# Kernel tuning notes

Measured on AMD Instinct MI355X. Metric: run time of the kernel, lower is better.

The kernel has to match this reference:

```python
import jax, jax.numpy as jnp
import numpy as np

K_CENTERS = 10
G_CENTERS = 2
EPS = 1e-12  # tf.math.l2_normalize epsilon


def setup_inputs() -> dict:
    key = jax.random.key(0)
    k1, k2, k3 = jax.random.split(key, 3)
    B, H, W, D = 16, 16, 64, 512
    KC = K_CENTERS + G_CENTERS
    feat = jax.random.normal(k1, (B, H, W, D), dtype=jnp.float32)
    cluster_score = jax.random.normal(k2, (B, H, W, KC), dtype=jnp.float32)
    cluster = jax.random.normal(k3, (KC, D), dtype=jnp.float32)
    return {"feat": feat, "cluster_score": cluster_score, "cluster": cluster}


def reference(feat, cluster_score, cluster):
    B, H, W, D = feat.shape
    KC = cluster.shape[0]
    # Softmax over clusters (stable)
    A = jax.nn.softmax(cluster_score, axis=-1)            # [B,H,W,KC]
    # Flatten spatial dims: sum_{s} A[b,s,k] * (feat[b,s,d] - cluster[k,d])
    Af = A.reshape(B, H * W, KC)
    ff = feat.reshape(B, H * W, D)
    # = einsum(A, feat) - (sum_s A)[b,k] * cluster[k,d]  (avoids [B,S,KC,D] intermediate)
    cluster_res = jnp.einsum('bsk,bsd->bkd', Af, ff) - Af.sum(axis=1)[..., None] * cluster[None]
    # GhostVLAD: keep only real clusters
    cluster_res = cluster_res[:, :K_CENTERS, :]           # [B,K,D]
    # L2 normalize over feature dim
    sq = jnp.sum(cluster_res * cluster_res, axis=-1, keepdims=True)
    cluster_l2 = cluster_res * jax.lax.rsqrt(jnp.maximum(sq, EPS))
    return cluster_l2.reshape(B, K_CENTERS * D)
```

## Files before the change

### kernel.cpp

```cpp
#include <hip/hip_runtime.h>


#define B_   16
#define S_   1024
#define D_   512
#define KC_  12
#define K_   10
#define CH_  16
#define SCH_ (S_ / CH_)
#define NT1  512
#define NPAR 4
#define NPX  (SCH_ / NPAR)

__global__ __launch_bounds__(NT1, 2) void vlad_accum(
    const float* __restrict__ feat, const float* __restrict__ score,
    float* __restrict__ part, float* __restrict__ asum_part)
{
    const int bid = blockIdx.x;
    const int b = bid / CH_, c = bid % CH_;
    const int s0 = c * SCH_;
    const int tid = threadIdx.x;
    const int par = tid >> 7;
    const int col = tid & 127;

    __shared__ float  As[SCH_][KC_];
    __shared__ float4 red[NPAR - 1][K_][128];

    float4 w0, w1, w2;
    if (tid < SCH_) {
        const float4* sp = (const float4*)(score + (size_t)(b * S_ + s0 + tid) * KC_);
        w0 = sp[0]; w1 = sp[1]; w2 = sp[2];
    }

    const float4* fp = (const float4*)(feat + (size_t)(b * S_ + s0) * D_) + col;
    float4 v[NPX];
    #pragma unroll
    for (int i = 0; i < NPX; i++)
        v[i] = fp[(size_t)(NPAR * i + par) * (D_ / 4)];

    if (tid < SCH_) {
        float x[KC_] = {w0.x, w0.y, w0.z, w0.w, w1.x, w1.y, w1.z, w1.w,
                        w2.x, w2.y, w2.z, w2.w};
        float m = x[0];
        #pragma unroll
        for (int k = 1; k < KC_; k++) m = fmaxf(m, x[k]);
        float sum = 0.f;
        #pragma unroll
        for (int k = 0; k < KC_; k++) { x[k] = __expf(x[k] - m); sum += x[k]; }
        const float inv = 1.0f / sum;
        #pragma unroll
        for (int k = 0; k < KC_; k++) {
            x[k] *= inv;
            As[tid][k] = x[k];
        }
        #pragma unroll
        for (int k = 0; k < K_; k++) {
            float r = x[k];
            #pragma unroll
            for (int off = 32; off > 0; off >>= 1) r += __shfl_down(r, off, 64);
            if (tid == 0) asum_part[(b * CH_ + c) * K_ + k] = r;
        }
    }
    __syncthreads();

    float acc[K_][4];
    #pragma unroll
    for (int k = 0; k < K_; k++)
        acc[k][0] = acc[k][1] = acc[k][2] = acc[k][3] = 0.f;

    #pragma unroll
    for (int i = 0; i < NPX; i++) {
        const int s = NPAR * i + par;
        const float4 a0 = *(const float4*)&As[s][0];
        const float4 a1 = *(const float4*)&As[s][4];
        const float2 a2 = *(const float2*)&As[s][8];
        const float a[K_] = {a0.x, a0.y, a0.z, a0.w, a1.x, a1.y, a1.z, a1.w,
                             a2.x, a2.y};
        #pragma unroll
        for (int k = 0; k < K_; k++) {
            acc[k][0] += a[k] * v[i].x;
            acc[k][1] += a[k] * v[i].y;
            acc[k][2] += a[k] * v[i].z;
            acc[k][3] += a[k] * v[i].w;
        }
    }

    if (par) {
        #pragma unroll
        for (int k = 0; k < K_; k++)
            red[par - 1][k][col] =
                make_float4(acc[k][0], acc[k][1], acc[k][2], acc[k][3]);
    }
    __syncthreads();
    if (!par) {
        float* pp = part + (((size_t)(b * K_) * CH_ + c) * D_) + col * 4;
        #pragma unroll
        for (int k = 0; k < K_; k++) {
            float v0 = acc[k][0], v1 = acc[k][1], v2 = acc[k][2], v3 = acc[k][3];
            #pragma unroll
            for (int p = 0; p < NPAR - 1; p++) {
                const float4 t = red[p][k][col];
                v0 += t.x; v1 += t.y; v2 += t.z; v3 += t.w;
            }
            *(float4*)(pp + (size_t)k * CH_ * D_) = make_float4(v0, v1, v2, v3);
        }
    }
}

__global__ __launch_bounds__(256) void vlad_final(
    const float* __restrict__ part, const float* __restrict__ asum_part,
    const float* __restrict__ cluster, float* __restrict__ out)
{
    const int b = blockIdx.x / K_;
    const int k = blockIdx.x % K_;
    const int tid = threadIdx.x;
    const int d = tid * 2;

    const float* base = part + ((size_t)(b * K_ + k) * CH_) * D_ + d;
    float2 v[CH_];
    #pragma unroll
    for (int c = 0; c < CH_; c++)
        v[c] = *(const float2*)(base + (size_t)c * D_);

    float asv = 0.f;
    #pragma unroll
    for (int c = 0; c < CH_; c++) asv += asum_part[(b * CH_ + c) * K_ + k];

    float s0 = 0.f, s1 = 0.f;
    #pragma unroll
    for (int c = 0; c < CH_; c++) { s0 += v[c].x; s1 += v[c].y; }

    const float2 cv = *(const float2*)(cluster + (size_t)k * D_ + d);
    const float r0 = s0 - asv * cv.x;
    const float r1 = s1 - asv * cv.y;

    float sq = r0 * r0 + r1 * r1;
    #pragma unroll
    for (int off = 32; off > 0; off >>= 1) sq += __shfl_down(sq, off, 64);
    __shared__ float wsum[4];
    if ((tid & 63) == 0) wsum[tid >> 6] = sq;
    __syncthreads();
    const float tot = wsum[0] + wsum[1] + wsum[2] + wsum[3];
    const float scale = rsqrtf(fmaxf(tot, 1e-12f));

    *(float2*)(out + (size_t)(b * K_ + k) * D_ + d) =
        make_float2(r0 * scale, r1 * scale);
}

extern "C" void kernel_launch(void* const* d_in, const int* in_sizes, int n_in,
                              void* d_out, int out_size, void* d_ws, size_t ws_size,
                              hipStream_t stream) {
    const float* feat    = (const float*)d_in[0];
    const float* score   = (const float*)d_in[1];
    const float* cluster = (const float*)d_in[2];
    float* out = (float*)d_out;

    float* part      = (float*)d_ws;
    float* asum_part = part + (size_t)B_ * K_ * CH_ * D_;

    vlad_accum<<<B_ * CH_, NT1, 0, stream>>>(feat, score, part, asum_part);
    vlad_final<<<B_ * K_, 256, 0, stream>>>(part, asum_part, cluster, out);
}
```

Before: 80.62 us.

## Fuse accumulate and finalize kernels via cooperative grid sync

Merges the two-kernel pipeline into a single cooperative kernel that runs the final reduction and L2 normalization after a grid-wide barrier. The blocking changes to 32 chunks of 256 threads per batch, giving 512 blocks, and the per-chunk cluster-weight sums are now computed serially from shared memory instead of by wave shuffles. The aim is to remove the second kernel launch and its gap. In exchange, cooperative launch overhead and the grid barrier may cost more than the launch they replace, and the partial buffer doubles in size, so the finalize step reads 32 partials per output.

```diff
diff --git a/kernel.cpp b/kernel.cpp
--- a/kernel.cpp
+++ b/kernel.cpp
@@ -1,4 +1,7 @@
 #include <hip/hip_runtime.h>
+#include <hip/hip_cooperative_groups.h>
+
+namespace cg = cooperative_groups;
 
 
 #define B_   16
@@ -6,37 +9,40 @@
 #define D_   512
 #define KC_  12
 #define K_   10
-#define CH_  16
+#define CH_  32
 #define SCH_ (S_ / CH_)
-#define NT1  512
-#define NPAR 4
+#define NT   256
+#define NPAR 2
 #define NPX  (SCH_ / NPAR)
 
-__global__ __launch_bounds__(NT1, 2) void vlad_accum(
+__global__ __launch_bounds__(NT, 2) void vlad_all(
     const float* __restrict__ feat, const float* __restrict__ score,
+    const float* __restrict__ cluster, float* __restrict__ out,
     float* __restrict__ part, float* __restrict__ asum_part)
 {
     const int bid = blockIdx.x;
-    const int b = bid / CH_, c = bid % CH_;
-    const int s0 = c * SCH_;
+    const int b   = bid >> 5;
+    const int c   = bid & (CH_ - 1);
+    const int s0  = c * SCH_;
     const int tid = threadIdx.x;
     const int par = tid >> 7;
     const int col = tid & 127;
 
     __shared__ float  As[SCH_][KC_];
-    __shared__ float4 red[NPAR - 1][K_][128];
+    __shared__ float4 red[K_][128];
+    __shared__ float  wsum[4];
 
     float4 w0, w1, w2;
     if (tid < SCH_) {
         const float4* sp = (const float4*)(score + (size_t)(b * S_ + s0 + tid) * KC_);
         w0 = sp[0]; w1 = sp[1]; w2 = sp[2];
     }
-
     const float4* fp = (const float4*)(feat + (size_t)(b * S_ + s0) * D_) + col;
     float4 v[NPX];
     #pragma unroll
     for (int i = 0; i < NPX; i++)
         v[i] = fp[(size_t)(NPAR * i + par) * (D_ / 4)];
+    __builtin_amdgcn_sched_barrier(0);
 
     if (tid < SCH_) {
         float x[KC_] = {w0.x, w0.y, w0.z, w0.w, w1.x, w1.y, w1.z, w1.w,
@@ -49,19 +55,16 @@
         for (int k = 0; k < KC_; k++) { x[k] = __expf(x[k] - m); sum += x[k]; }
         const float inv = 1.0f / sum;
         #pragma unroll
-        for (int k = 0; k < KC_; k++) {
-            x[k] *= inv;
-            As[tid][k] = x[k];
-        }
-        #pragma unroll
-        for (int k = 0; k < K_; k++) {
-            float r = x[k];
-            #pragma unroll
-            for (int off = 32; off > 0; off >>= 1) r += __shfl_down(r, off, 64);
-            if (tid == 0) asum_part[(b * CH_ + c) * K_ + k] = r;
-        }
+        for (int k = 0; k < KC_; k++) As[tid][k] = x[k] * inv;
     }
     __syncthreads();
+
+    if (tid < K_) {
+        float s = 0.f;
+        #pragma unroll
+        for (int p = 0; p < SCH_; p++) s += As[p][tid];
+        asum_part[(b * CH_ + c) * K_ + tid] = s;
+    }
 
     float acc[K_][4];
     #pragma unroll
@@ -71,9 +74,9 @@
     #pragma unroll
     for (int i = 0; i < NPX; i++) {
         const int s = NPAR * i + par;
-        const float4 a0 = *(const float4*)&As[s][0];
-        const float4 a1 = *(const float4*)&As[s][4];
-        const float2 a2 = *(const float2*)&As[s][8];
+        const float4 a0 = *(const float4*)(&As[s][0]);
+        const float4 a1 = *(const float4*)(&As[s][4]);
+        const float2 a2 = *(const float2*)(&As[s][8]);
         const float a[K_] = {a0.x, a0.y, a0.z, a0.w, a1.x, a1.y, a1.z, a1.w,
                              a2.x, a2.y};
         #pragma unroll
@@ -88,63 +91,61 @@
     if (par) {
         #pragma unroll
         for (int k = 0; k < K_; k++)
-            red[par - 1][k][col] =
-                make_float4(acc[k][0], acc[k][1], acc[k][2], acc[k][3]);
+            red[k][col] = make_float4(acc[k][0], acc[k][1], acc[k][2], acc[k][3]);
     }
     __syncthreads();
     if (!par) {
         float* pp = part + (((size_t)(b * K_) * CH_ + c) * D_) + col * 4;
         #pragma unroll
         for (int k = 0; k < K_; k++) {
-            float v0 = acc[k][0], v1 = acc[k][1], v2 = acc[k][2], v3 = acc[k][3];
-            #pragma unroll
-            for (int p = 0; p < NPAR - 1; p++) {
-                const float4 t = red[p][k][col];
-                v0 += t.x; v1 += t.y; v2 += t.z; v3 += t.w;
-            }
-            *(float4*)(pp + (size_t)k * CH_ * D_) = make_float4(v0, v1, v2, v3);
+            const float4 t = red[k][col];
+            *(float4*)(pp + (size_t)k * CH_ * D_) =
+                make_float4(acc[k][0] + t.x, acc[k][1] + t.y,
+                            acc[k][2] + t.z, acc[k][3] + t.w);
         }
     }
-}
 
-__global__ __launch_bounds__(256) void vlad_final(
-    const float* __restrict__ part, const float* __restrict__ asum_part,
-    const float* __restrict__ cluster, float* __restrict__ out)
-{
-    const int b = blockIdx.x / K_;
-    const int k = blockIdx.x % K_;
-    const int tid = threadIdx.x;
-    const int d = tid * 2;
+    __threadfence();
+    cg::this_grid().sync();
 
-    const float* base = part + ((size_t)(b * K_ + k) * CH_) * D_ + d;
-    float2 v[CH_];
-    #pragma unroll
-    for (int c = 0; c < CH_; c++)
-        v[c] = *(const float2*)(base + (size_t)c * D_);
+    if (bid < B_ * K_) {
+        const int b2 = bid / K_;
+        const int k2 = bid % K_;
+        const int d  = tid * 2;
+        const int lane = tid & 63, wave = tid >> 6;
 
-    float asv = 0.f;
-    #pragma unroll
-    for (int c = 0; c < CH_; c++) asv += asum_part[(b * CH_ + c) * K_ + k];
+        const float* base = part + ((size_t)(b2 * K_ + k2) * CH_) * D_ + d;
+        float2 pv[CH_];
+        #pragma unroll
+        for (int cc = 0; cc < CH_; cc++)
+            pv[cc] = *(const float2*)(base + (size_t)cc * D_);
+        __builtin_amdgcn_sched_barrier(0);
 
-    float s0 = 0.f, s1 = 0.f;
-    #pragma unroll
-    for (int c = 0; c < CH_; c++) { s0 += v[c].x; s1 += v[c].y; }
+        float asv = 0.f;
+        #pragma unroll
+        for (int cc = 0; cc < CH_; cc++)
+            asv += asum_part[(b2 * CH_ + cc) * K_ + k2];
 
-    const float2 cv = *(const float2*)(cluster + (size_t)k * D_ + d);
-    const float r0 = s0 - asv * cv.x;
-    const float r1 = s1 - asv * cv.y;
+        float r0 = 0.f, r1 = 0.f;
+        #pragma unroll
+        for (int cc = 0; cc < CH_; cc++) { r0 += pv[cc].x; r1 += pv[cc].y; }
 
-    float sq = r0 * r0 + r1 * r1;
-    #pragma unroll
-    for (int off = 32; off > 0; off >>= 1) sq += __shfl_down(sq, off, 64);
-    __shared__ float wsum[4];
-    if ((tid & 63) == 0) wsum[tid >> 6] = sq;
-    __syncthreads();
-    const float tot = wsum[0] + wsum[1] + wsum[2] + wsum[3];
-    const float scale = rsqrtf(fmaxf(tot, 1e-12f));
+        const float2 cv = *(const float2*)(cluster + (size_t)k2 * D_ + d);
+        r0 -= asv * cv.x;
+        r1 -= asv * cv.y;
 
-    *(float2*)(out + (size_t)(b * K_ + k) * D_ + d) =
-        make_float2(r0 * scale, r1 * scale);
+        float sq = r0 * r0 + r1 * r1;
+        #pragma unroll
+        for (int off = 32; off > 0; off >>= 1) sq += __shfl_down(sq, off, 64);
+        __syncthreads();
+        if (lane == 0) wsum[wave] = sq;
+        __syncthreads();
+        const float tot   = wsum[0] + wsum[1] + wsum[2] + wsum[3];
+        const float scale = rsqrtf(fmaxf(tot, 1e-12f));
+
+        *(float2*)(out + (size_t)(b2 * K_ + k2) * D_ + d) =
+            make_float2(r0 * scale, r1 * scale);
+    }
 }
 
 extern "C" void kernel_launch(void* const* d_in, const int* in_sizes, int n_in,
@@ -158,6 +159,8 @@
     float* part      = (float*)d_ws;
     float* asum_part = part + (size_t)B_ * K_ * CH_ * D_;
 
-    vlad_accum<<<B_ * CH_, NT1, 0, stream>>>(feat, score, part, asum_part);
-    vlad_final<<<B_ * K_, 256, 0, stream>>>(part, asum_part, cluster, out);
+    void* args[] = {(void*)&feat, (void*)&score, (void*)&cluster,
+                    (void*)&out,  (void*)&part,  (void*)&asum_part};
+    hipLaunchCooperativeKernel((const void*)vlad_all,
+                               dim3(B_ * CH_), dim3(NT), args, 0, stream);
 }
```

Result: slower. 185.6 us (+130.2%).

## Stage feature tiles into LDS via global_load_lds and drop cross-wave reduction

Applied to the files above, without the earlier changes.

The accumulation kernel now copies each block's feature chunk straight from global memory into shared memory with the async global_load_lds builtin, instead of loading it into registers. Every thread then walks all spatial rows for its own two feature columns. The spatial split doubles to 32 chunks with 256 threads per block, which removes the shared-memory cross-wave reduction and its extra barrier. In exchange, each block uses about 64KB of LDS, which limits occupancy, and the partial-sum buffer that the final kernel reads back doubles in size.

```diff
diff --git a/kernel.cpp b/kernel.cpp
--- a/kernel.cpp
+++ b/kernel.cpp
@@ -6,25 +6,24 @@
 #define D_   512
 #define KC_  12
 #define K_   10
-#define CH_  16
+#define CH_  32
 #define SCH_ (S_ / CH_)
-#define NT1  512
-#define NPAR 4
-#define NPX  (SCH_ / NPAR)
+#define NT1  256
 
 __global__ __launch_bounds__(NT1, 2) void vlad_accum(
     const float* __restrict__ feat, const float* __restrict__ score,
     float* __restrict__ part, float* __restrict__ asum_part)
 {
-    const int bid = blockIdx.x;
-    const int b = bid / CH_, c = bid % CH_;
-    const int s0 = c * SCH_;
-    const int tid = threadIdx.x;
-    const int par = tid >> 7;
-    const int col = tid & 127;
+    const int bid  = blockIdx.x;
+    const int b    = bid >> 5;
+    const int c    = bid & (CH_ - 1);
+    const int s0   = c * SCH_;
+    const int tid  = threadIdx.x;
+    const int wave = tid >> 6;
+    const int lane = tid & 63;
 
-    __shared__ float  As[SCH_][KC_];
-    __shared__ float4 red[NPAR - 1][K_][128];
+    __shared__ float fl[SCH_][D_];
+    __shared__ float As[SCH_][KC_];
 
     float4 w0, w1, w2;
     if (tid < SCH_) {
@@ -32,11 +31,19 @@
         w0 = sp[0]; w1 = sp[1]; w2 = sp[2];
     }
 
-    const float4* fp = (const float4*)(feat + (size_t)(b * S_ + s0) * D_) + col;
-    float4 v[NPX];
-    #pragma unroll
-    for (int i = 0; i < NPX; i++)
-        v[i] = fp[(size_t)(NPAR * i + par) * (D_ / 4)];
+    {
+        const float* gbase = feat + (size_t)(b * S_ + s0) * D_;
+        #pragma unroll
+        for (int j = 0; j < 16; j++) {
+            const int seg = wave * 16 + j;
+            const float* gp = gbase + seg * 256 + lane * 4;
+            const float* lp = &fl[0][0] + seg * 256;
+            __builtin_amdgcn_global_load_lds(
+                (const __attribute__((address_space(1))) void*)gp,
+                (__attribute__((address_space(3))) void*)lp,
+                16, 0, 0);
+        }
+    }
 
     if (tid < SCH_) {
         float x[KC_] = {w0.x, w0.y, w0.z, w0.w, w1.x, w1.y, w1.z, w1.w,
@@ -49,28 +56,31 @@
         for (int k = 0; k < KC_; k++) { x[k] = __expf(x[k] - m); sum += x[k]; }
         const float inv = 1.0f / sum;
         #pragma unroll
-        for (int k = 0; k < KC_; k++) {
-            x[k] *= inv;
-            As[tid][k] = x[k];
-        }
+        for (int k = 0; k < KC_; k++) x[k] *= inv;
+        *(float4*)&As[tid][0] = make_float4(x[0], x[1], x[2],  x[3]);
+        *(float4*)&As[tid][4] = make_float4(x[4], x[5], x[6],  x[7]);
+        *(float4*)&As[tid][8] = make_float4(x[8], x[9], x[10], x[11]);
         #pragma unroll
         for (int k = 0; k < K_; k++) {
             float r = x[k];
-            #pragma unroll
-            for (int off = 32; off > 0; off >>= 1) r += __shfl_down(r, off, 64);
+            r += __shfl_down(r, 16, 32);
+            r += __shfl_down(r, 8, 32);
+            r += __shfl_down(r, 4, 32);
+            r += __shfl_down(r, 2, 32);
+            r += __shfl_down(r, 1, 32);
             if (tid == 0) asum_part[(b * CH_ + c) * K_ + k] = r;
         }
     }
     __syncthreads();
 
-    float acc[K_][4];
+    const int d0 = tid * 2;
+    float acc[K_][2];
     #pragma unroll
-    for (int k = 0; k < K_; k++)
-        acc[k][0] = acc[k][1] = acc[k][2] = acc[k][3] = 0.f;
+    for (int k = 0; k < K_; k++) acc[k][0] = acc[k][1] = 0.f;
 
-    #pragma unroll
-    for (int i = 0; i < NPX; i++) {
-        const int s = NPAR * i + par;
+    #pragma unroll 8
+    for (int s = 0; s < SCH_; s++) {
+        const float2 v  = *(const float2*)&fl[s][d0];
         const float4 a0 = *(const float4*)&As[s][0];
         const float4 a1 = *(const float4*)&As[s][4];
         const float2 a2 = *(const float2*)&As[s][8];
@@ -78,57 +88,36 @@
                              a2.x, a2.y};
         #pragma unroll
         for (int k = 0; k < K_; k++) {
-            acc[k][0] += a[k] * v[i].x;
-            acc[k][1] += a[k] * v[i].y;
-            acc[k][2] += a[k] * v[i].z;
-            acc[k][3] += a[k] * v[i].w;
+            acc[k][0] += a[k] * v.x;
+            acc[k][1] += a[k] * v.y;
         }
     }
 
-    if (par) {
-        #pragma unroll
-        for (int k = 0; k < K_; k++)
-            red[par - 1][k][col] =
-                make_float4(acc[k][0], acc[k][1], acc[k][2], acc[k][3]);
-    }
-    __syncthreads();
-    if (!par) {
-        float* pp = part + (((size_t)(b * K_) * CH_ + c) * D_) + col * 4;
-        #pragma unroll
-        for (int k = 0; k < K_; k++) {
-            float v0 = acc[k][0], v1 = acc[k][1], v2 = acc[k][2], v3 = acc[k][3];
-            #pragma unroll
-            for (int p = 0; p < NPAR - 1; p++) {
-                const float4 t = red[p][k][col];
-                v0 += t.x; v1 += t.y; v2 += t.z; v3 += t.w;
-            }
-            *(float4*)(pp + (size_t)k * CH_ * D_) = make_float4(v0, v1, v2, v3);
-        }
-    }
+    float* pp = part + (((size_t)(b * K_) * CH_ + c) * D_) + d0;
+    #pragma unroll
+    for (int k = 0; k < K_; k++)
+        *(float2*)(pp + (size_t)k * CH_ * D_) = make_float2(acc[k][0], acc[k][1]);
 }
 
 __global__ __launch_bounds__(256) void vlad_final(
     const float* __restrict__ part, const float* __restrict__ asum_part,
     const float* __restrict__ cluster, float* __restrict__ out)
 {
-    const int b = blockIdx.x / K_;
-    const int k = blockIdx.x % K_;
+    const int b   = blockIdx.x / K_;
+    const int k   = blockIdx.x % K_;
     const int tid = threadIdx.x;
-    const int d = tid * 2;
+    const int d   = tid * 2;
 
     const float* base = part + ((size_t)(b * K_ + k) * CH_) * D_ + d;
-    float2 v[CH_];
+    float s0 = 0.f, s1 = 0.f;
     #pragma unroll
-    for (int c = 0; c < CH_; c++)
-        v[c] = *(const float2*)(base + (size_t)c * D_);
-
+    for (int c = 0; c < CH_; c++) {
+        const float2 v = *(const float2*)(base + (size_t)c * D_);
+        s0 += v.x; s1 += v.y;
+    }
     float asv = 0.f;
     #pragma unroll
     for (int c = 0; c < CH_; c++) asv += asum_part[(b * CH_ + c) * K_ + k];
-
-    float s0 = 0.f, s1 = 0.f;
-    #pragma unroll
-    for (int c = 0; c < CH_; c++) { s0 += v[c].x; s1 += v[c].y; }
 
     const float2 cv = *(const float2*)(cluster + (size_t)k * D_ + d);
     const float r0 = s0 - asv * cv.x;
@@ -140,7 +129,7 @@
     __shared__ float wsum[4];
     if ((tid & 63) == 0) wsum[tid >> 6] = sq;
     __syncthreads();
-    const float tot = wsum[0] + wsum[1] + wsum[2] + wsum[3];
+    const float tot   = wsum[0] + wsum[1] + wsum[2] + wsum[3];
     const float scale = rsqrtf(fmaxf(tot, 1e-12f));
 
     *(float2*)(out + (size_t)(b * K_ + k) * D_ + d) =
```

Result: slower. 85.15 us (+5.6%).

## Double spatial chunk count, stream feat loads, and parallelize final reduction

Applied to the files above, without the earlier changes.

Splits each batch's spatial range into 32 chunks instead of 16. The accumulate kernel now launches 512 blocks and has a higher occupancy bound. Feature rows are loaded inside the FMA loop instead of being preloaded into a register array, which cuts register pressure. The final kernel uses 512 threads with float4 loads: four thread groups each sum 8 chunk partials, combine them through shared memory, and then L2-normalize. This trades better latency hiding and GPU fill against twice as much partial-sum traffic through the workspace.

```diff
diff --git a/kernel.cpp b/kernel.cpp
--- a/kernel.cpp
+++ b/kernel.cpp
@@ -6,19 +6,20 @@
 #define D_   512
 #define KC_  12
 #define K_   10
-#define CH_  16
+#define CH_  32
 #define SCH_ (S_ / CH_)
-#define NT1  512
+#define NT   512
 #define NPAR 4
 #define NPX  (SCH_ / NPAR)
 
-__global__ __launch_bounds__(NT1, 2) void vlad_accum(
+__global__ __launch_bounds__(NT, 4) void vlad_accum(
     const float* __restrict__ feat, const float* __restrict__ score,
     float* __restrict__ part, float* __restrict__ asum_part)
 {
     const int bid = blockIdx.x;
-    const int b = bid / CH_, c = bid % CH_;
-    const int s0 = c * SCH_;
+    const int b   = bid >> 5;
+    const int c   = bid & (CH_ - 1);
+    const int s0  = c * SCH_;
     const int tid = threadIdx.x;
     const int par = tid >> 7;
     const int col = tid & 127;
@@ -26,19 +27,9 @@
     __shared__ float  As[SCH_][KC_];
     __shared__ float4 red[NPAR - 1][K_][128];
 
-    float4 w0, w1, w2;
     if (tid < SCH_) {
         const float4* sp = (const float4*)(score + (size_t)(b * S_ + s0 + tid) * KC_);
-        w0 = sp[0]; w1 = sp[1]; w2 = sp[2];
-    }
-
-    const float4* fp = (const float4*)(feat + (size_t)(b * S_ + s0) * D_) + col;
-    float4 v[NPX];
-    #pragma unroll
-    for (int i = 0; i < NPX; i++)
-        v[i] = fp[(size_t)(NPAR * i + par) * (D_ / 4)];
-
-    if (tid < SCH_) {
+        const float4 w0 = sp[0], w1 = sp[1], w2 = sp[2];
         float x[KC_] = {w0.x, w0.y, w0.z, w0.w, w1.x, w1.y, w1.z, w1.w,
                         w2.x, w2.y, w2.z, w2.w};
         float m = x[0];
@@ -49,20 +40,24 @@
         for (int k = 0; k < KC_; k++) { x[k] = __expf(x[k] - m); sum += x[k]; }
         const float inv = 1.0f / sum;
         #pragma unroll
-        for (int k = 0; k < KC_; k++) {
-            x[k] *= inv;
-            As[tid][k] = x[k];
-        }
+        for (int k = 0; k < KC_; k++) x[k] *= inv;
+        *(float4*)&As[tid][0] = make_float4(x[0], x[1], x[2],  x[3]);
+        *(float4*)&As[tid][4] = make_float4(x[4], x[5], x[6],  x[7]);
+        *(float4*)&As[tid][8] = make_float4(x[8], x[9], x[10], x[11]);
         #pragma unroll
         for (int k = 0; k < K_; k++) {
             float r = x[k];
-            #pragma unroll
-            for (int off = 32; off > 0; off >>= 1) r += __shfl_down(r, off, 64);
+            r += __shfl_down(r, 16, 32);
+            r += __shfl_down(r, 8, 32);
+            r += __shfl_down(r, 4, 32);
+            r += __shfl_down(r, 2, 32);
+            r += __shfl_down(r, 1, 32);
             if (tid == 0) asum_part[(b * CH_ + c) * K_ + k] = r;
         }
     }
     __syncthreads();
 
+    const float4* fp = (const float4*)(feat + (size_t)(b * S_ + s0) * D_) + col;
     float acc[K_][4];
     #pragma unroll
     for (int k = 0; k < K_; k++)
@@ -70,7 +65,8 @@
 
     #pragma unroll
     for (int i = 0; i < NPX; i++) {
-        const int s = NPAR * i + par;
+        const int s = i * NPAR + par;
+        const float4 v  = fp[(size_t)s * 128];
         const float4 a0 = *(const float4*)&As[s][0];
         const float4 a1 = *(const float4*)&As[s][4];
         const float2 a2 = *(const float2*)&As[s][8];
@@ -78,10 +74,10 @@
                              a2.x, a2.y};
         #pragma unroll
         for (int k = 0; k < K_; k++) {
-            acc[k][0] += a[k] * v[i].x;
-            acc[k][1] += a[k] * v[i].y;
-            acc[k][2] += a[k] * v[i].z;
-            acc[k][3] += a[k] * v[i].w;
+            acc[k][0] += a[k] * v.x;
+            acc[k][1] += a[k] * v.y;
+            acc[k][2] += a[k] * v.z;
+            acc[k][3] += a[k] * v.w;
         }
     }
 
@@ -107,44 +103,66 @@
     }
 }
 
-__global__ __launch_bounds__(256) void vlad_final(
+__global__ __launch_bounds__(NT, 4) void vlad_final(
     const float* __restrict__ part, const float* __restrict__ asum_part,
     const float* __restrict__ cluster, float* __restrict__ out)
 {
-    const int b = blockIdx.x / K_;
-    const int k = blockIdx.x % K_;
-    const int tid = threadIdx.x;
-    const int d = tid * 2;
+    const int b    = blockIdx.x / K_;
+    const int k    = blockIdx.x % K_;
+    const int tid  = threadIdx.x;
+    const int cg   = tid >> 7;
+    const int dcol = tid & 127;
+    const int lane = tid & 63;
+    const int wave = tid >> 6;
 
-    const float* base = part + ((size_t)(b * K_ + k) * CH_) * D_ + d;
-    float2 v[CH_];
+    __shared__ float4 red2[3][128];
+    __shared__ float  asumS;
+    __shared__ float  wsum2[2];
+
+    const float4* base =
+        (const float4*)(part + (((size_t)(b * K_ + k) * CH_) + cg * 8) * D_) + dcol;
+    float4 a = make_float4(0.f, 0.f, 0.f, 0.f);
     #pragma unroll
-    for (int c = 0; c < CH_; c++)
-        v[c] = *(const float2*)(base + (size_t)c * D_);
+    for (int cc = 0; cc < 8; cc++) {
+        const float4 v = base[(size_t)cc * 128];
+        a.x += v.x; a.y += v.y; a.z += v.z; a.w += v.w;
+    }
 
-    float asv = 0.f;
-    #pragma unroll
-    for (int c = 0; c < CH_; c++) asv += asum_part[(b * CH_ + c) * K_ + k];
+    if (tid < 32) {
+        float r = asum_part[(b * CH_ + tid) * K_ + k];
+        r += __shfl_down(r, 16, 32);
+        r += __shfl_down(r, 8, 32);
+        r += __shfl_down(r, 4, 32);
+        r += __shfl_down(r, 2, 32);
+        r += __shfl_down(r, 1, 32);
+        if (tid == 0) asumS = r;
+    }
 
-    float s0 = 0.f, s1 = 0.f;
-    #pragma unroll
-    for (int c = 0; c < CH_; c++) { s0 += v[c].x; s1 += v[c].y; }
+    if (cg) red2[cg - 1][dcol] = a;
+    __syncthreads();
 
-    const float2 cv = *(const float2*)(cluster + (size_t)k * D_ + d);
-    const float r0 = s0 - asv * cv.x;
-    const float r1 = s1 - asv * cv.y;
-
-    float sq = r0 * r0 + r1 * r1;
-    #pragma unroll
-    for (int off = 32; off > 0; off >>= 1) sq += __shfl_down(sq, off, 64);
-    __shared__ float wsum[4];
-    if ((tid & 63) == 0) wsum[tid >> 6] = sq;
+    float4 r4;
+    float  sq = 0.f;
+    if (!cg) {
+        const float4 r0 = red2[0][dcol], r1 = red2[1][dcol], r2 = red2[2][dcol];
+        const float4 cv = ((const float4*)(cluster + (size_t)k * D_))[dcol];
+        const float asv = asumS;
+        r4.x = a.x + r0.x + r1.x + r2.x - asv * cv.x;
+        r4.y = a.y + r0.y + r1.y + r2.y - asv * cv.y;
+        r4.z = a.z + r0.z + r1.z + r2.z - asv * cv.z;
+        r4.w = a.w + r0.w + r1.w + r2.w - asv * cv.w;
+        sq = r4.x * r4.x + r4.y * r4.y + r4.z * r4.z + r4.w * r4.w;
+        #pragma unroll
+        for (int off = 32; off > 0; off >>= 1) sq += __shfl_down(sq, off, 64);
+        if (lane == 0) wsum2[wave] = sq;
+    }
     __syncthreads();
-    const float tot = wsum[0] + wsum[1] + wsum[2] + wsum[3];
-    const float scale = rsqrtf(fmaxf(tot, 1e-12f));
-
-    *(float2*)(out + (size_t)(b * K_ + k) * D_ + d) =
-        make_float2(r0 * scale, r1 * scale);
+    if (!cg) {
+        const float tot   = wsum2[0] + wsum2[1];
+        const float scale = rsqrtf(fmaxf(tot, 1e-12f));
+        ((float4*)(out + (size_t)(b * K_ + k) * D_))[dcol] =
+            make_float4(r4.x * scale, r4.y * scale, r4.z * scale, r4.w * scale);
+    }
 }
 
 extern "C" void kernel_launch(void* const* d_in, const int* in_sizes, int n_in,
@@ -158,6 +176,6 @@
     float* part      = (float*)d_ws;
     float* asum_part = part + (size_t)B_ * K_ * CH_ * D_;
 
-    vlad_accum<<<B_ * CH_, NT1, 0, stream>>>(feat, score, part, asum_part);
-    vlad_final<<<B_ * K_, 256, 0, stream>>>(part, asum_part, cluster, out);
+    vlad_accum<<<B_ * CH_, NT, 0, stream>>>(feat, score, part, asum_part);
+    vlad_final<<<B_ * K_, NT, 0, stream>>>(part, asum_part, cluster, out);
 }
```

New measurement: 82.38 us. 2.2% more time.
